# Kernel tuning notes

Measured on AMD Instinct MI355X. Metric: run time of the kernel, lower is better.

Reference implementation:

```python
import jax, jax.numpy as jnp
import numpy as np

N = 100000   # nodes
E = 800000   # directed edges
IN = 256     # in_channels (== hidden, required by repo's vn MLP dims)
HID = 256    # hidden_channels
OUT = 40     # out_channels (arxiv classes)
EPS = 1e-5


def setup_inputs() -> dict:
    key = jax.random.key(0)
    ks = jax.random.split(key, 8)
    def nrm(k, shape, scale=0.05):
        return jax.random.normal(k, shape, dtype=jnp.float32) * scale
    return {
        "x": nrm(ks[0], (N, IN), 1.0),
        "edge_index": jax.random.randint(ks[1], (2, E), 0, N, dtype=jnp.int32),
        # GCNConv weights (PyG: x @ W, then normalized aggregation, then + bias)
        "W0": nrm(ks[2], (IN, HID)),  "b0": jnp.zeros((HID,), jnp.float32),
        "W1": nrm(ks[3], (HID, HID)), "b1": jnp.zeros((HID,), jnp.float32),
        "W2": nrm(ks[4], (HID, OUT)), "b2": jnp.zeros((OUT,), jnp.float32),
        # BatchNorm1d affine params (batch-stat math, training mode)
        "bn_g0": jnp.ones((HID,), jnp.float32), "bn_b0": jnp.zeros((HID,), jnp.float32),
        "bn_g1": jnp.ones((HID,), jnp.float32), "bn_b1": jnp.zeros((HID,), jnp.float32),
        # virtual node embedding (init to 0 per reset_parameters)
        "vn_emb": jnp.zeros((1, IN), jnp.float32),
        # mlp_vns[0]: Linear(IN,HID) + LayerNorm(HID) + ReLU
        "vn_W0": nrm(ks[5], (IN, HID)),  "vn_b0": jnp.zeros((HID,), jnp.float32),
        "ln_g0": jnp.ones((HID,), jnp.float32), "ln_b0": jnp.zeros((HID,), jnp.float32),
        # mlp_vns[1]: Linear(HID,HID) + LayerNorm(HID) + ReLU
        "vn_W1": nrm(ks[6], (HID, HID)), "vn_b1": jnp.zeros((HID,), jnp.float32),
        "ln_g1": jnp.ones((HID,), jnp.float32), "ln_b1": jnp.zeros((HID,), jnp.float32),
    }


def _forward(x, edge_index, W0, b0, W1, b1, W2, b2, bn_g0, bn_b0, bn_g1, bn_b1,
             vn_emb, vn_W0, vn_b0, ln_g0, ln_b0, vn_W1, vn_b1, ln_g1, ln_b1):
    src, dst = edge_index[0], edge_index[1]
    # GCN symmetric normalization with self-loops: deg = in-degree + 1
    deg = jax.ops.segment_sum(jnp.ones(src.shape, jnp.float32), dst, num_segments=N) + 1.0
    dis = jax.lax.rsqrt(deg)                       # deg^{-1/2}  [N]
    coef = (dis[src] * dis[dst])[:, None]          # edge norm   [E,1]
    self_coef = (dis * dis)[:, None]               # self-loop norm = deg^{-1}  [N,1]

    def gcn(h, W, b):
        h = h @ W                                             # [N, out]
        agg = jax.ops.segment_sum(h[src] * coef, dst, num_segments=N)
        return agg + h * self_coef + b

    def bn(h, g, bv):  # BatchNorm1d, batch statistics over nodes
        mu = h.mean(0)
        var = ((h - mu) ** 2).mean(0)
        return (h - mu) * jax.lax.rsqrt(var + EPS) * g + bv

    def ln(h, g, bv):  # LayerNorm over last dim
        mu = h.mean(-1, keepdims=True)
        var = ((h - mu) ** 2).mean(-1, keepdims=True)
        return (h - mu) * jax.lax.rsqrt(var + EPS) * g + bv

    vx = vn_emb                                   # [1, IN]
    # layer 0
    h = x + vx                                    # virtual-node broadcast
    h = gcn(h, W0, b0)
    h = jax.nn.relu(bn(h, bn_g0, bn_b0))          # dropout = identity (eval)
    pool = jnp.sum(h, axis=0, keepdims=True)      # global_add_pool
    vx = jax.nn.relu(ln((pool + vx) @ vn_W0 + vn_b0, ln_g0, ln_b0))
    # layer 1
    h = h + vx
    h = gcn(h, W1, b1)
    h = jax.nn.relu(bn(h, bn_g1, bn_b1))
    pool = jnp.sum(h, axis=0, keepdims=True)
    vx = jax.nn.relu(ln((pool + vx) @ vn_W1 + vn_b1, ln_g1, ln_b1))
    # layer 2 (output)
    h = h + vx
    h = gcn(h, W2, b2)
    return jax.nn.log_softmax(h, axis=-1)


def reference(x, edge_index, W0, b0, W1, b1, W2, b2, bn_g0, bn_b0, bn_g1, bn_b1,
              vn_emb, vn_W0, vn_b0, ln_g0, ln_b0, vn_W1, vn_b1, ln_g1, ln_b1):
    return _forward(x, edge_index, W0, b0, W1, b1, W2, b2, bn_g0, bn_b0, bn_g1, bn_b1,
                    vn_emb, vn_W0, vn_b0, ln_g0, ln_b0, vn_W1, vn_b1, ln_g1, ln_b1)
```

## Files before the change

kernel.cpp:

```cpp
#include <hip/hip_runtime.h>
#include <hip/hip_bf16.h>
#include <cstdint>

#define N_NODES 100000
#define N_EDGES 800000
#define CH      256
#define COUT    40
#define COUTP   48
#define EPS     1e-5f
#define SCAN_CHUNK 1024
#define NSCAN_BLK  98
#define AGG_NPW 16

typedef unsigned short u16;
typedef unsigned int   u32;
typedef short s16x8 __attribute__((ext_vector_type(8)));
typedef float f32x4 __attribute__((ext_vector_type(4)));

__device__ __forceinline__ float b2f(u32 u) { return __uint_as_float(u << 16); }
__device__ __forceinline__ u16 f2b(float f) {
    u32 u = __float_as_uint(f);
    u32 r = (u + 0x7fffu + ((u >> 16) & 1u)) >> 16;
    return (u16)r;
}
__device__ __forceinline__ u32 packb(float a, float b) {
    return (u32)f2b(a) | ((u32)f2b(b) << 16);
}
__device__ __forceinline__ void unpack8(uint4 v, float* f) {
    f[0] = b2f(v.x & 0xffffu); f[1] = b2f(v.x >> 16);
    f[2] = b2f(v.y & 0xffffu); f[3] = b2f(v.y >> 16);
    f[4] = b2f(v.z & 0xffffu); f[5] = b2f(v.z >> 16);
    f[6] = b2f(v.w & 0xffffu); f[7] = b2f(v.w >> 16);
}

__global__ void k_count(const int* __restrict__ dst, int* __restrict__ counts) {
    int e = blockIdx.x * 256 + threadIdx.x;
    if (e < N_EDGES) atomicAdd(&counts[dst[e]], 1);
}

__global__ void k_scan1(const int* __restrict__ counts, int* __restrict__ partial,
                        int* __restrict__ blocksums) {
    __shared__ int sdata[256];
    int base = blockIdx.x * SCAN_CHUNK;
    int t = threadIdx.x;
    int v[4]; int s = 0;
    for (int j = 0; j < 4; j++) {
        int i = base + t * 4 + j;
        v[j] = (i < N_NODES) ? counts[i] : 0;
        s += v[j];
    }
    sdata[t] = s; __syncthreads();
    for (int off = 1; off < 256; off <<= 1) {
        int x = (t >= off) ? sdata[t - off] : 0;
        __syncthreads();
        sdata[t] += x;
        __syncthreads();
    }
    int incl = sdata[t];
    int run = incl - s;
    if (t == 255) blocksums[blockIdx.x] = incl;
    for (int j = 0; j < 4; j++) {
        int i = base + t * 4 + j;
        if (i < N_NODES) partial[i] = run;
        run += v[j];
    }
}

__global__ void k_scan2(int* __restrict__ blocksums) {
    __shared__ int sd[128];
    int t = threadIdx.x;
    int v = (t < NSCAN_BLK) ? blocksums[t] : 0;
    sd[t] = v; __syncthreads();
    for (int off = 1; off < 128; off <<= 1) {
        int x = (t >= off) ? sd[t - off] : 0;
        __syncthreads();
        sd[t] += x;
        __syncthreads();
    }
    if (t < NSCAN_BLK) blocksums[t] = sd[t] - v;
}

__global__ void k_scan3(int* __restrict__ row_start, const int* __restrict__ blocksums,
                        int* __restrict__ cursor, const int* __restrict__ counts,
                        float* __restrict__ dis) {
    int i = blockIdx.x * 256 + threadIdx.x;
    if (i < N_NODES) {
        int v = row_start[i] + blocksums[i >> 10];
        row_start[i] = v;
        cursor[i] = v;
        dis[i] = rsqrtf(1.0f + (float)counts[i]);
    }
}

__global__ void k_fill(const int* __restrict__ src, const int* __restrict__ dst,
                       int* __restrict__ cursor, int2* __restrict__ edata,
                       const float* __restrict__ dis) {
    int e = blockIdx.x * 256 + threadIdx.x;
    if (e < N_EDGES) {
        int d = dst[e], s = src[e];
        int p = atomicAdd(&cursor[d], 1);
        int2 v; v.x = s; v.y = __float_as_int(dis[s] * dis[d]);
        edata[p] = v;
    }
}

__global__ void k_wt3(const float* __restrict__ W0, const float* __restrict__ W1,
                      const float* __restrict__ W2,
                      u16* __restrict__ T0, u16* __restrict__ T1, u16* __restrict__ T2) {
    int b = blockIdx.x, k = threadIdx.x;
    if (b < 256) {
        T0[b * 256 + k] = f2b(W0[k * 256 + b]);
    } else if (b < 512) {
        int n = b - 256;
        T1[n * 256 + k] = f2b(W1[k * 256 + n]);
    } else {
        int n = b - 512;
        T2[n * 256 + k] = f2b(n < COUT ? W2[k * COUT + n] : 0.f);
    }
}

__global__ void k_vecmat(const float* __restrict__ vec, const float* __restrict__ W,
                         int ncols, int npad, float* __restrict__ outv) {
    __shared__ float s[256];
    int t = threadIdx.x;
    s[t] = vec[t];
    __syncthreads();
    float acc = 0.f;
    if (t < ncols) {
        for (int k = 0; k < 256; k++) acc += s[k] * W[k * ncols + t];
    }
    if (t < npad) outv[t] = acc;
}

__global__ __launch_bounds__(256) void k_gemm_f32a(const float* __restrict__ A,
                                                   const u16* __restrict__ Wt,
                                                   u16* __restrict__ Hout) {
    __shared__ u16 Bs[256 * 72];
    __shared__ u16 As[64 * 72];
    const int t = threadIdx.x;
    const int wave = t >> 6, lane = t & 63;
    const int lm = lane & 15, quad = lane >> 4;
    const int m0 = blockIdx.x * 64;
    const int ar = t >> 2, as_ = (t & 3) * 16;
    const int arow = m0 + ar;
    const f32x4 vz = {0.f, 0.f, 0.f, 0.f};
    f32x4 acc[4][4];
    for (int m = 0; m < 4; m++)
        for (int c = 0; c < 4; c++) acc[m][c] = vz;

    for (int k0 = 0; k0 < 256; k0 += 64) {
        {
            const uint4* bsrc = (const uint4*)(Wt + t * 256 + k0);
            uint4* bdst = (uint4*)(Bs + t * 72);
#pragma unroll
            for (int j = 0; j < 8; j++) bdst[j] = bsrc[j];
            uint4 p0 = {0,0,0,0}, p1 = {0,0,0,0};
            if (arow < N_NODES) {
                const float4* asrc = (const float4*)(A + (size_t)arow * 256 + k0 + as_);
                float4 x0 = asrc[0], x1 = asrc[1], x2 = asrc[2], x3 = asrc[3];
                p0.x = packb(x0.x, x0.y); p0.y = packb(x0.z, x0.w);
                p0.z = packb(x1.x, x1.y); p0.w = packb(x1.z, x1.w);
                p1.x = packb(x2.x, x2.y); p1.y = packb(x2.z, x2.w);
                p1.z = packb(x3.x, x3.y); p1.w = packb(x3.z, x3.w);
            }
            uint4* adst = (uint4*)(As + ar * 72 + as_);
            adst[0] = p0; adst[1] = p1;
        }
        __syncthreads();
#pragma unroll
        for (int kk = 0; kk < 64; kk += 32) {
            s16x8 af[4], bf[4];
#pragma unroll
            for (int m = 0; m < 4; m++)
                af[m] = *(const s16x8*)(As + (m * 16 + lm) * 72 + kk + quad * 8);
#pragma unroll
            for (int c = 0; c < 4; c++)
                bf[c] = *(const s16x8*)(Bs + (wave * 64 + c * 16 + lm) * 72 + kk + quad * 8);
#pragma unroll
            for (int c = 0; c < 4; c++)
#pragma unroll
                for (int m = 0; m < 4; m++)
                    acc[m][c] = __builtin_amdgcn_mfma_f32_16x16x32_bf16(af[m], bf[c], acc[m][c], 0, 0, 0);
        }
        __syncthreads();
    }
#pragma unroll
    for (int m = 0; m < 4; m++) {
#pragma unroll
        for (int c = 0; c < 4; c++) {
            int col = wave * 64 + c * 16 + lm;
#pragma unroll
            for (int i = 0; i < 4; i++) {
                int row = m0 + m * 16 + quad * 4 + i;
                if (row < N_NODES) Hout[(size_t)row * 256 + col] = f2b(acc[m][c][i]);
            }
        }
    }
}

__global__ __launch_bounds__(256) void k_gemm_bn(const u16* __restrict__ A,
                                                 const float* __restrict__ stats,
                                                 const float* __restrict__ g,
                                                 const float* __restrict__ bv,
                                                 const u16* __restrict__ Wt,
                                                 u16* __restrict__ Hout,
                                                 float* __restrict__ pool) {
    __shared__ u16 Bs[256 * 72];
    __shared__ u16 As[64 * 72];
    __shared__ float ggs[256], bcs[256], pls[256];
    const int t = threadIdx.x;
    const int wave = t >> 6, lane = t & 63;
    const int lm = lane & 15, quad = lane >> 4;
    const int m0 = blockIdx.x * 64;
    const int ar = t >> 2, as_ = (t & 3) * 16;
    const int arow = m0 + ar;
    {
        const float inv = 1.0f / (float)N_NODES;
        float mu = stats[t] * inv;
        float var = stats[256 + t] * inv - mu * mu;
        float rs = rsqrtf(var + EPS);
        float gg = g[t] * rs;
        ggs[t] = gg; bcs[t] = bv[t] - mu * gg;
        pls[t] = 0.f;
    }
    __syncthreads();
    const f32x4 vz = {0.f, 0.f, 0.f, 0.f};
    f32x4 acc[4][4];
    for (int m = 0; m < 4; m++)
        for (int c = 0; c < 4; c++) acc[m][c] = vz;

    for (int k0 = 0; k0 < 256; k0 += 64) {
        {
            const uint4* bsrc = (const uint4*)(Wt + t * 256 + k0);
            uint4* bdst = (uint4*)(Bs + t * 72);
#pragma unroll
            for (int j = 0; j < 8; j++) bdst[j] = bsrc[j];
            float f[16];
            if (arow < N_NODES) {
                const uint4* asrc = (const uint4*)(A + (size_t)arow * 256 + k0 + as_);
                uint4 r0 = asrc[0], r1 = asrc[1];
                unpack8(r0, f); unpack8(r1, f + 8);
#pragma unroll
                for (int j = 0; j < 16; j++) {
                    int c = k0 + as_ + j;
                    f[j] = fmaxf(f[j] * ggs[c] + bcs[c], 0.f);
                }
            } else {
#pragma unroll
                for (int j = 0; j < 16; j++) f[j] = 0.f;
            }
#pragma unroll
            for (int j = 0; j < 16; j++) {
                float v = f[j];
                v += __shfl_xor(v, 4);  v += __shfl_xor(v, 8);
                v += __shfl_xor(v, 16); v += __shfl_xor(v, 32);
                if (lane < 4) atomicAdd(&pls[k0 + lane * 16 + j], v);
            }
            uint4 p0, p1;
            p0.x = packb(f[0], f[1]);   p0.y = packb(f[2], f[3]);
            p0.z = packb(f[4], f[5]);   p0.w = packb(f[6], f[7]);
            p1.x = packb(f[8], f[9]);   p1.y = packb(f[10], f[11]);
            p1.z = packb(f[12], f[13]); p1.w = packb(f[14], f[15]);
            uint4* adst = (uint4*)(As + ar * 72 + as_);
            adst[0] = p0; adst[1] = p1;
        }
        __syncthreads();
#pragma unroll
        for (int kk = 0; kk < 64; kk += 32) {
            s16x8 af[4], bf[4];
#pragma unroll
            for (int m = 0; m < 4; m++)
                af[m] = *(const s16x8*)(As + (m * 16 + lm) * 72 + kk + quad * 8);
#pragma unroll
            for (int c = 0; c < 4; c++)
                bf[c] = *(const s16x8*)(Bs + (wave * 64 + c * 16 + lm) * 72 + kk + quad * 8);
#pragma unroll
            for (int c = 0; c < 4; c++)
#pragma unroll
                for (int m = 0; m < 4; m++)
                    acc[m][c] = __builtin_amdgcn_mfma_f32_16x16x32_bf16(af[m], bf[c], acc[m][c], 0, 0, 0);
        }
        __syncthreads();
    }
    atomicAdd(&pool[(blockIdx.x & 7) * 256 + t], pls[t]);
#pragma unroll
    for (int m = 0; m < 4; m++) {
#pragma unroll
        for (int c = 0; c < 4; c++) {
            int col = wave * 64 + c * 16 + lm;
#pragma unroll
            for (int i = 0; i < 4; i++) {
                int row = m0 + m * 16 + quad * 4 + i;
                if (row < N_NODES) Hout[(size_t)row * 256 + col] = f2b(acc[m][c][i]);
            }
        }
    }
}

__global__ __launch_bounds__(256) void k_gemm2_bn(const u16* __restrict__ A,
                                                  const float* __restrict__ stats,
                                                  const float* __restrict__ g,
                                                  const float* __restrict__ bv,
                                                  const u16* __restrict__ Wt,
                                                  u16* __restrict__ Hout,
                                                  float* __restrict__ pool) {
    __shared__ u16 Bs[48 * 72];
    __shared__ u16 As[64 * 72];
    __shared__ float ggs[256], bcs[256], pls[256];
    const int t = threadIdx.x;
    const int wave = t >> 6, lane = t & 63;
    const int lm = lane & 15, quad = lane >> 4;
    const int m0 = blockIdx.x * 64;
    const int ar = t >> 2, as_ = (t & 3) * 16;
    const int arow = m0 + ar;
    {
        const float inv = 1.0f / (float)N_NODES;
        float mu = stats[t] * inv;
        float var = stats[256 + t] * inv - mu * mu;
        float rs = rsqrtf(var + EPS);
        float gg = g[t] * rs;
        ggs[t] = gg; bcs[t] = bv[t] - mu * gg;
        pls[t] = 0.f;
    }
    __syncthreads();
    const f32x4 vz = {0.f, 0.f, 0.f, 0.f};
    f32x4 acc[3]; acc[0] = vz; acc[1] = vz; acc[2] = vz;

    for (int k0 = 0; k0 < 256; k0 += 64) {
        {
            if (t < 48) {
                const uint4* bsrc = (const uint4*)(Wt + t * 256 + k0);
                uint4* bdst = (uint4*)(Bs + t * 72);
#pragma unroll
                for (int j = 0; j < 8; j++) bdst[j] = bsrc[j];
            }
            float f[16];
            if (arow < N_NODES) {
                const uint4* asrc = (const uint4*)(A + (size_t)arow * 256 + k0 + as_);
                uint4 r0 = asrc[0], r1 = asrc[1];
                unpack8(r0, f); unpack8(r1, f + 8);
#pragma unroll
                for (int j = 0; j < 16; j++) {
                    int c = k0 + as_ + j;
                    f[j] = fmaxf(f[j] * ggs[c] + bcs[c], 0.f);
                }
            } else {
#pragma unroll
                for (int j = 0; j < 16; j++) f[j] = 0.f;
            }
#pragma unroll
            for (int j = 0; j < 16; j++) {
                float v = f[j];
                v += __shfl_xor(v, 4);  v += __shfl_xor(v, 8);
                v += __shfl_xor(v, 16); v += __shfl_xor(v, 32);
                if (lane < 4) atomicAdd(&pls[k0 + lane * 16 + j], v);
            }
            uint4 p0, p1;
            p0.x = packb(f[0], f[1]);   p0.y = packb(f[2], f[3]);
            p0.z = packb(f[4], f[5]);   p0.w = packb(f[6], f[7]);
            p1.x = packb(f[8], f[9]);   p1.y = packb(f[10], f[11]);
            p1.z = packb(f[12], f[13]); p1.w = packb(f[14], f[15]);
            uint4* adst = (uint4*)(As + ar * 72 + as_);
            adst[0] = p0; adst[1] = p1;
        }
        __syncthreads();
#pragma unroll
        for (int kk = 0; kk < 64; kk += 32) {
            s16x8 af = *(const s16x8*)(As + (wave * 16 + lm) * 72 + kk + quad * 8);
#pragma unroll
            for (int c = 0; c < 3; c++) {
                s16x8 bf = *(const s16x8*)(Bs + (c * 16 + lm) * 72 + kk + quad * 8);
                acc[c] = __builtin_amdgcn_mfma_f32_16x16x32_bf16(af, bf, acc[c], 0, 0, 0);
            }
        }
        __syncthreads();
    }
    atomicAdd(&pool[(blockIdx.x & 7) * 256 + t], pls[t]);
#pragma unroll
    for (int c = 0; c < 3; c++) {
        int col = c * 16 + lm;
#pragma unroll
        for (int i = 0; i < 4; i++) {
            int row = m0 + wave * 16 + quad * 4 + i;
            if (row < N_NODES) Hout[(size_t)row * COUTP + col] = f2b(acc[c][i]);
        }
    }
}

__global__ __launch_bounds__(256) void k_agg(const u16* __restrict__ H2,
                                             const int* __restrict__ row_start,
                                             const int* __restrict__ counts,
                                             const int2* __restrict__ edata,
                                             const float* __restrict__ dis,
                                             const float* __restrict__ bias,
                                             const float* __restrict__ v2,
                                             u16* __restrict__ OutB,
                                             float* __restrict__ stats) {
    __shared__ float ls[512];
    const int t = threadIdx.x, wave = t >> 6, lane = t & 63;
    const int half = lane >> 5, hl = lane & 31;
    const int ci = hl * 8;
    const float4 bbA = *(const float4*)(bias + ci);
    const float4 bbB = *(const float4*)(bias + ci + 4);
    const float4 vvA = *(const float4*)(v2 + ci);
    const float4 vvB = *(const float4*)(v2 + ci + 4);
    float s[8], q[8];
#pragma unroll
    for (int j = 0; j < 8; j++) { s[j] = 0.f; q[j] = 0.f; }

    const int nbase = blockIdx.x * (4 * AGG_NPW) + wave * AGG_NPW;
    const int nid = nbase + lane;
    const bool nv = (lane < AGG_NPW) && (nid < N_NODES);
    const int   my_rs = nv ? row_start[nid] : 0;
    const int   my_ct = nv ? counts[nid] : 0;
    const float my_dn = nv ? dis[nid] : 0.f;

    int beg = __shfl(my_rs, 0), cnt = __shfl(my_ct, 0);
    int2 my_e = {0, 0};
    if (lane < cnt) my_e = edata[beg + lane];

    for (int i = 0; i < AGG_NPW; i++) {
        const int node = nbase + i;
        if (node >= N_NODES) break;
        const int2 cur_e = my_e;
        const int  ccnt = cnt, cbeg = beg;
        const float dn = __shfl(my_dn, i);
        const uint4 rs_ = *(const uint4*)(H2 + (size_t)node * 256 + ci);
        if (i + 1 < AGG_NPW && node + 1 < N_NODES) {
            beg = __shfl(my_rs, i + 1);
            cnt = __shfl(my_ct, i + 1);
            int2 tmp = {0, 0};
            if (lane < cnt) tmp = edata[beg + lane];
            my_e = tmp;
        }
        const int cnt64 = ccnt < 64 ? ccnt : 64;
        const int cnt8 = (cnt64 + 7) & ~7;
        float a[8];
#pragma unroll
        for (int j = 0; j < 8; j++) a[j] = 0.f;
        float cs = 0.f;
        for (int e = 0; e < cnt8; e += 8) {
            const int   si0 = __shfl(cur_e.x, e + half);
            const int   si1 = __shfl(cur_e.x, e + 2 + half);
            const int   si2 = __shfl(cur_e.x, e + 4 + half);
            const int   si3 = __shfl(cur_e.x, e + 6 + half);
            const float cf0 = __int_as_float(__shfl(cur_e.y, e + half));
            const float cf1 = __int_as_float(__shfl(cur_e.y, e + 2 + half));
            const float cf2 = __int_as_float(__shfl(cur_e.y, e + 4 + half));
            const float cf3 = __int_as_float(__shfl(cur_e.y, e + 6 + half));
            const uint4 r0 = *(const uint4*)(H2 + (size_t)si0 * 256 + ci);
            const uint4 r1 = *(const uint4*)(H2 + (size_t)si1 * 256 + ci);
            const uint4 r2 = *(const uint4*)(H2 + (size_t)si2 * 256 + ci);
            const uint4 r3 = *(const uint4*)(H2 + (size_t)si3 * 256 + ci);
            cs += cf0 + cf1 + cf2 + cf3;
            a[0] += cf0*b2f(r0.x&0xffffu) + cf1*b2f(r1.x&0xffffu) + cf2*b2f(r2.x&0xffffu) + cf3*b2f(r3.x&0xffffu);
            a[1] += cf0*b2f(r0.x>>16)     + cf1*b2f(r1.x>>16)     + cf2*b2f(r2.x>>16)     + cf3*b2f(r3.x>>16);
            a[2] += cf0*b2f(r0.y&0xffffu) + cf1*b2f(r1.y&0xffffu) + cf2*b2f(r2.y&0xffffu) + cf3*b2f(r3.y&0xffffu);
            a[3] += cf0*b2f(r0.y>>16)     + cf1*b2f(r1.y>>16)     + cf2*b2f(r2.y>>16)     + cf3*b2f(r3.y>>16);
            a[4] += cf0*b2f(r0.z&0xffffu) + cf1*b2f(r1.z&0xffffu) + cf2*b2f(r2.z&0xffffu) + cf3*b2f(r3.z&0xffffu);
            a[5] += cf0*b2f(r0.z>>16)     + cf1*b2f(r1.z>>16)     + cf2*b2f(r2.z>>16)     + cf3*b2f(r3.z>>16);
            a[6] += cf0*b2f(r0.w&0xffffu) + cf1*b2f(r1.w&0xffffu) + cf2*b2f(r2.w&0xffffu) + cf3*b2f(r3.w&0xffffu);
            a[7] += cf0*b2f(r0.w>>16)     + cf1*b2f(r1.w>>16)     + cf2*b2f(r2.w>>16)     + cf3*b2f(r3.w>>16);
        }
        if (ccnt > 64) {
            int e2 = 64;
            for (; e2 + 2 <= ccnt; e2 += 2) {
                const int2 ed_ = edata[cbeg + e2 + half];
                const float cf = __int_as_float(ed_.y);
                const uint4 r = *(const uint4*)(H2 + (size_t)ed_.x * 256 + ci);
                cs += cf;
                a[0] += cf*b2f(r.x&0xffffu); a[1] += cf*b2f(r.x>>16);
                a[2] += cf*b2f(r.y&0xffffu); a[3] += cf*b2f(r.y>>16);
                a[4] += cf*b2f(r.z&0xffffu); a[5] += cf*b2f(r.z>>16);
                a[6] += cf*b2f(r.w&0xffffu); a[7] += cf*b2f(r.w>>16);
            }
            if (e2 < ccnt && half == 0) {
                const int2 ed_ = edata[cbeg + e2];
                const float cf = __int_as_float(ed_.y);
                const uint4 r = *(const uint4*)(H2 + (size_t)ed_.x * 256 + ci);
                cs += cf;
                a[0] += cf*b2f(r.x&0xffffu); a[1] += cf*b2f(r.x>>16);
                a[2] += cf*b2f(r.y&0xffffu); a[3] += cf*b2f(r.y>>16);
                a[4] += cf*b2f(r.z&0xffffu); a[5] += cf*b2f(r.z>>16);
                a[6] += cf*b2f(r.w&0xffffu); a[7] += cf*b2f(r.w>>16);
            }
        }
        cs += __shfl_xor(cs, 32);
#pragma unroll
        for (int j = 0; j < 8; j++) a[j] += __shfl_xor(a[j], 32);
        const float sc = dn * dn, cv = cs + sc;
        const float f0 = a[0] + sc*b2f(rs_.x&0xffffu) + cv*vvA.x + bbA.x;
        const float f1 = a[1] + sc*b2f(rs_.x>>16)     + cv*vvA.y + bbA.y;
        const float f2 = a[2] + sc*b2f(rs_.y&0xffffu) + cv*vvA.z + bbA.z;
        const float f3 = a[3] + sc*b2f(rs_.y>>16)     + cv*vvA.w + bbA.w;
        const float f4 = a[4] + sc*b2f(rs_.z&0xffffu) + cv*vvB.x + bbB.x;
        const float f5 = a[5] + sc*b2f(rs_.z>>16)     + cv*vvB.y + bbB.y;
        const float f6 = a[6] + sc*b2f(rs_.w&0xffffu) + cv*vvB.z + bbB.z;
        const float f7 = a[7] + sc*b2f(rs_.w>>16)     + cv*vvB.w + bbB.w;
        if (half == 0) {
            uint4 o;
            o.x = packb(f0, f1); o.y = packb(f2, f3);
            o.z = packb(f4, f5); o.w = packb(f6, f7);
            *(uint4*)(OutB + (size_t)node * 256 + ci) = o;
        }
        s[0] += f0; q[0] += f0*f0;  s[1] += f1; q[1] += f1*f1;
        s[2] += f2; q[2] += f2*f2;  s[3] += f3; q[3] += f3*f3;
        s[4] += f4; q[4] += f4*f4;  s[5] += f5; q[5] += f5*f5;
        s[6] += f6; q[6] += f6*f6;  s[7] += f7; q[7] += f7*f7;
    }
    ls[t] = 0.f; ls[256 + t] = 0.f;
    __syncthreads();
    if (half == 0) {
#pragma unroll
        for (int j = 0; j < 8; j++) {
            atomicAdd(&ls[ci + j], s[j]);
            atomicAdd(&ls[256 + ci + j], q[j]);
        }
    }
    __syncthreads();
    atomicAdd(&stats[t], ls[t]);
    atomicAdd(&stats[256 + t], ls[256 + t]);
}

__global__ void k_vx(const float* __restrict__ pool, const float* __restrict__ vx_old,
                     const float* __restrict__ vnW, const float* __restrict__ vnb,
                     const float* __restrict__ lng, const float* __restrict__ lnb,
                     float* __restrict__ vx_new,
                     const float* __restrict__ Wnext, int ncn, int npn,
                     float* __restrict__ v2n) {
    __shared__ float s[256];
    __shared__ float red[256];
    int t = threadIdx.x;
    float pv = 0.f;
#pragma unroll
    for (int r = 0; r < 8; r++) pv += pool[r * 256 + t];
    s[t] = pv + vx_old[t];
    __syncthreads();
    float y = vnb[t];
    for (int k = 0; k < 256; k++) y += s[k] * vnW[k * 256 + t];
    red[t] = y; __syncthreads();
    for (int off = 128; off > 0; off >>= 1) {
        if (t < off) red[t] += red[t + off];
        __syncthreads();
    }
    float mu = red[0] * (1.f / 256.f);
    __syncthreads();
    float d = y - mu;
    red[t] = d * d; __syncthreads();
    for (int off = 128; off > 0; off >>= 1) {
        if (t < off) red[t] += red[t + off];
        __syncthreads();
    }
    float var = red[0] * (1.f / 256.f);
    float v = fmaxf(d * rsqrtf(var + EPS) * lng[t] + lnb[t], 0.f);
    vx_new[t] = v;
    __syncthreads();
    s[t] = v;
    __syncthreads();
    float acc = 0.f;
    if (t < ncn) {
        for (int k = 0; k < 256; k++) acc += s[k] * Wnext[k * ncn + t];
    }
    if (t < npn) v2n[t] = acc;
}

__global__ __launch_bounds__(256) void k_agg2(const u16* __restrict__ H2,
                                              const int* __restrict__ row_start,
                                              const int* __restrict__ counts,
                                              const int2* __restrict__ edata,
                                              const float* __restrict__ dis,
                                              const float* __restrict__ bias,
                                              const float* __restrict__ v2,
                                              float* __restrict__ OutF) {
    const int t = threadIdx.x, wave = t >> 6, lane = t & 63;
    const int half = lane >> 5, hl = lane & 31;
    const bool gact = hl < 24;
    const bool cact = hl < 20;
    const int c0 = 2 * hl;
    float bb0 = 0.f, bb1 = 0.f, vv0 = 0.f, vv1 = 0.f;
    if (cact) {
        float2 bv = *(const float2*)(bias + c0); bb0 = bv.x; bb1 = bv.y;
        float2 vvv = *(const float2*)(v2 + c0);  vv0 = vvv.x; vv1 = vvv.y;
    }
    const int nbase = blockIdx.x * 16 + wave * 4;
    for (int i = 0; i < 4; i++) {
        const int node = nbase + i;
        const int beg = row_start[node], cnt = counts[node];
        const float dn = dis[node];
        float a0 = 0.f, a1 = 0.f, cs = 0.f;
        int e = half;
        for (; e + 6 < cnt; e += 8) {
            int2 ea = edata[beg+e],   eb = edata[beg+e+2];
            int2 ec = edata[beg+e+4], ed = edata[beg+e+6];
            float ca = __int_as_float(ea.y), cb = __int_as_float(eb.y);
            float cc = __int_as_float(ec.y), cd = __int_as_float(ed.y);
            u32 ra = 0, rb = 0, rc = 0, rd = 0;
            if (gact) {
                ra = *(const u32*)(H2 + (size_t)ea.x * COUTP + c0);
                rb = *(const u32*)(H2 + (size_t)eb.x * COUTP + c0);
                rc = *(const u32*)(H2 + (size_t)ec.x * COUTP + c0);
                rd = *(const u32*)(H2 + (size_t)ed.x * COUTP + c0);
            }
            cs += ca + cb + cc + cd;
            a0 += ca*b2f(ra&0xffffu) + cb*b2f(rb&0xffffu) + cc*b2f(rc&0xffffu) + cd*b2f(rd&0xffffu);
            a1 += ca*b2f(ra>>16)     + cb*b2f(rb>>16)     + cc*b2f(rc>>16)     + cd*b2f(rd>>16);
        }
        for (; e < cnt; e += 2) {
            int2 ea = edata[beg+e];
            float ca = __int_as_float(ea.y);
            u32 ra = gact ? *(const u32*)(H2 + (size_t)ea.x * COUTP + c0) : 0u;
            cs += ca;
            a0 += ca*b2f(ra&0xffffu); a1 += ca*b2f(ra>>16);
        }
        a0 += __shfl_xor(a0, 32);
        a1 += __shfl_xor(a1, 32);
        cs += __shfl_xor(cs, 32);
        const float sc = dn * dn;
        u32 rs_ = gact ? *(const u32*)(H2 + (size_t)node * COUTP + c0) : 0u;
        float h0 = a0 + sc*b2f(rs_&0xffffu) + (cs+sc)*vv0 + bb0;
        float h1 = a1 + sc*b2f(rs_>>16)     + (cs+sc)*vv1 + bb1;
        float m = cact ? fmaxf(h0, h1) : -3.0e38f;
#pragma unroll
        for (int off = 16; off > 0; off >>= 1) m = fmaxf(m, __shfl_xor(m, off));
        float ex = cact ? (expf(h0 - m) + expf(h1 - m)) : 0.f;
        float se = ex;
#pragma unroll
        for (int off = 16; off > 0; off >>= 1) se += __shfl_xor(se, off);
        float lg = logf(se);
        if (cact && half == 0) {
            float2 o = {h0 - m - lg, h1 - m - lg};
            *(float2*)(OutF + (size_t)node * COUT + c0) = o;
        }
    }
}

extern "C" void kernel_launch(void* const* d_in, const int* in_sizes, int n_in,
                              void* d_out, int out_size, void* d_ws, size_t ws_size,
                              hipStream_t stream) {
    const float* x   = (const float*)d_in[0];
    const int*   ei  = (const int*)d_in[1];
    const int*   esrc = ei;
    const int*   edst = ei + N_EDGES;
    const float* W0 = (const float*)d_in[2];  const float* b0 = (const float*)d_in[3];
    const float* W1 = (const float*)d_in[4];  const float* b1 = (const float*)d_in[5];
    const float* W2 = (const float*)d_in[6];  const float* b2 = (const float*)d_in[7];
    const float* bg0 = (const float*)d_in[8]; const float* bb0 = (const float*)d_in[9];
    const float* bg1 = (const float*)d_in[10]; const float* bb1 = (const float*)d_in[11];
    const float* vn_emb = (const float*)d_in[12];
    const float* vW0 = (const float*)d_in[13]; const float* vb0 = (const float*)d_in[14];
    const float* lg0 = (const float*)d_in[15]; const float* lb0 = (const float*)d_in[16];
    const float* vW1 = (const float*)d_in[17]; const float* vb1 = (const float*)d_in[18];
    const float* lg1 = (const float*)d_in[19]; const float* lb1 = (const float*)d_in[20];

    char* w = (char*)d_ws;
    auto alloc = [&](size_t bytes) { void* p = (void*)w; w += ((bytes + 255) / 256) * 256; return p; };
    u16* H2    = (u16*)alloc((size_t)N_NODES * 256 * 2);
    u16* OutB  = (u16*)alloc((size_t)N_NODES * 256 * 2);
    int2* edata = (int2*)alloc((size_t)N_EDGES * 8);
    int* counts = (int*)alloc((size_t)N_NODES * 4);
    int* rowst  = (int*)alloc((size_t)N_NODES * 4);
    int* cursor = (int*)alloc((size_t)N_NODES * 4);
    float* dis  = (float*)alloc((size_t)N_NODES * 4);
    u16* Wtb0 = (u16*)alloc(256 * 256 * 2);
    u16* Wtb1 = (u16*)alloc(256 * 256 * 2);
    u16* Wt2b = (u16*)alloc(COUTP * 256 * 2);
    int* scanblk = (int*)alloc(128 * 4);
    float* statsA = (float*)alloc(2560 * 4);
    float* statsB = (float*)alloc(2560 * 4);
    float* vxA = (float*)alloc(256 * 4);
    float* vxB = (float*)alloc(256 * 4);
    float* v20 = (float*)alloc(256 * 4);
    float* v21 = (float*)alloc(256 * 4);
    float* v22 = (float*)alloc(64 * 4);
    (void)ws_size; (void)in_sizes; (void)n_in; (void)out_size;

    hipMemsetAsync(counts, 0, (size_t)N_NODES * 4, stream);
    hipMemsetAsync(statsA, 0, 2560 * 4, stream);
    hipMemsetAsync(statsB, 0, 2560 * 4, stream);
    k_count<<<(N_EDGES + 255) / 256, 256, 0, stream>>>(edst, counts);
    k_scan1<<<NSCAN_BLK, 256, 0, stream>>>(counts, rowst, scanblk);
    k_scan2<<<1, 128, 0, stream>>>(scanblk);
    k_scan3<<<(N_NODES + 255) / 256, 256, 0, stream>>>(rowst, scanblk, cursor, counts, dis);
    k_fill<<<(N_EDGES + 255) / 256, 256, 0, stream>>>(esrc, edst, cursor, edata, dis);

    k_wt3<<<512 + COUTP, 256, 0, stream>>>(W0, W1, W2, Wtb0, Wtb1, Wt2b);
    k_vecmat<<<1, 256, 0, stream>>>(vn_emb, W0, 256, 256, v20);

    const int gemmblk = (N_NODES + 63) / 64;
    const int aggblk = (N_NODES + 63) / 64;

    k_gemm_f32a<<<gemmblk, 256, 0, stream>>>(x, Wtb0, H2);
    k_agg<<<aggblk, 256, 0, stream>>>(H2, rowst, counts, edata, dis, b0, v20, OutB, statsA);
    k_gemm_bn<<<gemmblk, 256, 0, stream>>>(OutB, statsA, bg0, bb0, Wtb1, H2, statsA + 512);
    k_vx<<<1, 256, 0, stream>>>(statsA + 512, vn_emb, vW0, vb0, lg0, lb0, vxA, W1, 256, 256, v21);
    k_agg<<<aggblk, 256, 0, stream>>>(H2, rowst, counts, edata, dis, b1, v21, OutB, statsB);
    k_gemm2_bn<<<gemmblk, 256, 0, stream>>>(OutB, statsB, bg1, bb1, Wt2b, H2, statsB + 512);
    k_vx<<<1, 256, 0, stream>>>(statsB + 512, vxA, vW1, vb1, lg1, lb1, vxB, W2, COUT, COUTP, v22);
    k_agg2<<<N_NODES / 16, 256, 0, stream>>>(H2, rowst, counts, edata, dis, b2, v22, (float*)d_out);
}
```

Measured before the change: 735.6 us.

## Make aggregation kernel persistent with atomic ticket-based dynamic node scheduling

The two hidden-layer aggregation kernels now run as a fixed grid of 2048 persistent blocks. Each wave claims 4-node chunks from a global atomic ticket counter instead of owning a static 16-node range, which is meant to even out the load imbalance caused by varying node degrees. Launch bounds now request 8 waves per SIMD, and the per-block BN statistic atomics happen once per persistent block rather than once per small block. The cost is one global atomic per chunk, shorter prefetch pipelining across nodes, and a ticket buffer that must be zeroed on every call.

Result: slower. 1.493 ms (+103.0%).

```diff
diff --git a/kernel.cpp b/kernel.cpp
--- a/kernel.cpp
+++ b/kernel.cpp
@@ -10,7 +10,8 @@
 #define EPS     1e-5f
 #define SCAN_CHUNK 1024
 #define NSCAN_BLK  98
-#define AGG_NPW 16
+#define AGG_CHUNK  4
+#define AGG_BLOCKS 2048
 
 typedef unsigned short u16;
 typedef unsigned int   u32;
@@ -387,7 +388,7 @@
     }
 }
 
-__global__ __launch_bounds__(256) void k_agg(const u16* __restrict__ H2,
+__global__ __launch_bounds__(256, 8) void k_agg(const u16* __restrict__ H2,
                                              const int* __restrict__ row_start,
                                              const int* __restrict__ counts,
                                              const int2* __restrict__ edata,
@@ -395,9 +396,10 @@
                                              const float* __restrict__ bias,
                                              const float* __restrict__ v2,
                                              u16* __restrict__ OutB,
-                                             float* __restrict__ stats) {
+                                             float* __restrict__ stats,
+                                             int* __restrict__ ticket) {
     __shared__ float ls[512];
-    const int t = threadIdx.x, wave = t >> 6, lane = t & 63;
+    const int t = threadIdx.x, lane = t & 63;
     const int half = lane >> 5, hl = lane & 31;
     const int ci = hl * 8;
     const float4 bbA = *(const float4*)(bias + ci);
@@ -408,105 +410,110 @@
 #pragma unroll
     for (int j = 0; j < 8; j++) { s[j] = 0.f; q[j] = 0.f; }
 
-    const int nbase = blockIdx.x * (4 * AGG_NPW) + wave * AGG_NPW;
-    const int nid = nbase + lane;
-    const bool nv = (lane < AGG_NPW) && (nid < N_NODES);
-    const int   my_rs = nv ? row_start[nid] : 0;
-    const int   my_ct = nv ? counts[nid] : 0;
-    const float my_dn = nv ? dis[nid] : 0.f;
-
-    int beg = __shfl(my_rs, 0), cnt = __shfl(my_ct, 0);
-    int2 my_e = {0, 0};
-    if (lane < cnt) my_e = edata[beg + lane];
-
-    for (int i = 0; i < AGG_NPW; i++) {
-        const int node = nbase + i;
-        if (node >= N_NODES) break;
-        const int2 cur_e = my_e;
-        const int  ccnt = cnt, cbeg = beg;
-        const float dn = __shfl(my_dn, i);
-        const uint4 rs_ = *(const uint4*)(H2 + (size_t)node * 256 + ci);
-        if (i + 1 < AGG_NPW && node + 1 < N_NODES) {
-            beg = __shfl(my_rs, i + 1);
-            cnt = __shfl(my_ct, i + 1);
-            int2 tmp = {0, 0};
-            if (lane < cnt) tmp = edata[beg + lane];
-            my_e = tmp;
-        }
-        const int cnt64 = ccnt < 64 ? ccnt : 64;
-        const int cnt8 = (cnt64 + 7) & ~7;
-        float a[8];
-#pragma unroll
-        for (int j = 0; j < 8; j++) a[j] = 0.f;
-        float cs = 0.f;
-        for (int e = 0; e < cnt8; e += 8) {
-            const int   si0 = __shfl(cur_e.x, e + half);
-            const int   si1 = __shfl(cur_e.x, e + 2 + half);
-            const int   si2 = __shfl(cur_e.x, e + 4 + half);
-            const int   si3 = __shfl(cur_e.x, e + 6 + half);
-            const float cf0 = __int_as_float(__shfl(cur_e.y, e + half));
-            const float cf1 = __int_as_float(__shfl(cur_e.y, e + 2 + half));
-            const float cf2 = __int_as_float(__shfl(cur_e.y, e + 4 + half));
-            const float cf3 = __int_as_float(__shfl(cur_e.y, e + 6 + half));
-            const uint4 r0 = *(const uint4*)(H2 + (size_t)si0 * 256 + ci);
-            const uint4 r1 = *(const uint4*)(H2 + (size_t)si1 * 256 + ci);
-            const uint4 r2 = *(const uint4*)(H2 + (size_t)si2 * 256 + ci);
-            const uint4 r3 = *(const uint4*)(H2 + (size_t)si3 * 256 + ci);
-            cs += cf0 + cf1 + cf2 + cf3;
-            a[0] += cf0*b2f(r0.x&0xffffu) + cf1*b2f(r1.x&0xffffu) + cf2*b2f(r2.x&0xffffu) + cf3*b2f(r3.x&0xffffu);
-            a[1] += cf0*b2f(r0.x>>16)     + cf1*b2f(r1.x>>16)     + cf2*b2f(r2.x>>16)     + cf3*b2f(r3.x>>16);
-            a[2] += cf0*b2f(r0.y&0xffffu) + cf1*b2f(r1.y&0xffffu) + cf2*b2f(r2.y&0xffffu) + cf3*b2f(r3.y&0xffffu);
-            a[3] += cf0*b2f(r0.y>>16)     + cf1*b2f(r1.y>>16)     + cf2*b2f(r2.y>>16)     + cf3*b2f(r3.y>>16);
-            a[4] += cf0*b2f(r0.z&0xffffu) + cf1*b2f(r1.z&0xffffu) + cf2*b2f(r2.z&0xffffu) + cf3*b2f(r3.z&0xffffu);
-            a[5] += cf0*b2f(r0.z>>16)     + cf1*b2f(r1.z>>16)     + cf2*b2f(r2.z>>16)     + cf3*b2f(r3.z>>16);
-            a[6] += cf0*b2f(r0.w&0xffffu) + cf1*b2f(r1.w&0xffffu) + cf2*b2f(r2.w&0xffffu) + cf3*b2f(r3.w&0xffffu);
-            a[7] += cf0*b2f(r0.w>>16)     + cf1*b2f(r1.w>>16)     + cf2*b2f(r2.w>>16)     + cf3*b2f(r3.w>>16);
-        }
-        if (ccnt > 64) {
-            int e2 = 64;
-            for (; e2 + 2 <= ccnt; e2 += 2) {
-                const int2 ed_ = edata[cbeg + e2 + half];
-                const float cf = __int_as_float(ed_.y);
-                const uint4 r = *(const uint4*)(H2 + (size_t)ed_.x * 256 + ci);
-                cs += cf;
-                a[0] += cf*b2f(r.x&0xffffu); a[1] += cf*b2f(r.x>>16);
-                a[2] += cf*b2f(r.y&0xffffu); a[3] += cf*b2f(r.y>>16);
-                a[4] += cf*b2f(r.z&0xffffu); a[5] += cf*b2f(r.z>>16);
-                a[6] += cf*b2f(r.w&0xffffu); a[7] += cf*b2f(r.w>>16);
-            }
-            if (e2 < ccnt && half == 0) {
-                const int2 ed_ = edata[cbeg + e2];
-                const float cf = __int_as_float(ed_.y);
-                const uint4 r = *(const uint4*)(H2 + (size_t)ed_.x * 256 + ci);
-                cs += cf;
-                a[0] += cf*b2f(r.x&0xffffu); a[1] += cf*b2f(r.x>>16);
-                a[2] += cf*b2f(r.y&0xffffu); a[3] += cf*b2f(r.y>>16);
-                a[4] += cf*b2f(r.z&0xffffu); a[5] += cf*b2f(r.z>>16);
-                a[6] += cf*b2f(r.w&0xffffu); a[7] += cf*b2f(r.w>>16);
-            }
-        }
-        cs += __shfl_xor(cs, 32);
-#pragma unroll
-        for (int j = 0; j < 8; j++) a[j] += __shfl_xor(a[j], 32);
-        const float sc = dn * dn, cv = cs + sc;
-        const float f0 = a[0] + sc*b2f(rs_.x&0xffffu) + cv*vvA.x + bbA.x;
-        const float f1 = a[1] + sc*b2f(rs_.x>>16)     + cv*vvA.y + bbA.y;
-        const float f2 = a[2] + sc*b2f(rs_.y&0xffffu) + cv*vvA.z + bbA.z;
-        const float f3 = a[3] + sc*b2f(rs_.y>>16)     + cv*vvA.w + bbA.w;
-        const float f4 = a[4] + sc*b2f(rs_.z&0xffffu) + cv*vvB.x + bbB.x;
-        const float f5 = a[5] + sc*b2f(rs_.z>>16)     + cv*vvB.y + bbB.y;
-        const float f6 = a[6] + sc*b2f(rs_.w&0xffffu) + cv*vvB.z + bbB.z;
-        const float f7 = a[7] + sc*b2f(rs_.w>>16)     + cv*vvB.w + bbB.w;
-        if (half == 0) {
-            uint4 o;
-            o.x = packb(f0, f1); o.y = packb(f2, f3);
-            o.z = packb(f4, f5); o.w = packb(f6, f7);
-            *(uint4*)(OutB + (size_t)node * 256 + ci) = o;
-        }
-        s[0] += f0; q[0] += f0*f0;  s[1] += f1; q[1] += f1*f1;
-        s[2] += f2; q[2] += f2*f2;  s[3] += f3; q[3] += f3*f3;
-        s[4] += f4; q[4] += f4*f4;  s[5] += f5; q[5] += f5*f5;
-        s[6] += f6; q[6] += f6*f6;  s[7] += f7; q[7] += f7*f7;
+    for (;;) {
+        int tk = 0;
+        if (lane == 0) tk = atomicAdd(ticket, AGG_CHUNK);
+        const int nbase = __shfl(tk, 0);
+        if (nbase >= N_NODES) break;
+        const int nid = nbase + lane;
+        const bool nv = (lane < AGG_CHUNK) && (nid < N_NODES);
+        const int   my_rs = nv ? row_start[nid] : 0;
+        const int   my_ct = nv ? counts[nid] : 0;
+        const float my_dn = nv ? dis[nid] : 0.f;
+
+        int beg = __shfl(my_rs, 0), cnt = __shfl(my_ct, 0);
+        int2 my_e = {0, 0};
+        if (lane < cnt) my_e = edata[beg + lane];
+
+        for (int i = 0; i < AGG_CHUNK; i++) {
+            const int node = nbase + i;
+            if (node >= N_NODES) break;
+            const int2 cur_e = my_e;
+            const int  ccnt = cnt, cbeg = beg;
+            const float dn = __shfl(my_dn, i);
+            const uint4 rs_ = *(const uint4*)(H2 + (size_t)node * 256 + ci);
+            if (i + 1 < AGG_CHUNK && node + 1 < N_NODES) {
+                beg = __shfl(my_rs, i + 1);
+                cnt = __shfl(my_ct, i + 1);
+                int2 tmp = {0, 0};
+                if (lane < cnt) tmp = edata[beg + lane];
+                my_e = tmp;
+            }
+            const int cnt64 = ccnt < 64 ? ccnt : 64;
+            const int cnt8 = (cnt64 + 7) & ~7;
+            float a[8];
+#pragma unroll
+            for (int j = 0; j < 8; j++) a[j] = 0.f;
+            float cs = 0.f;
+            for (int e = 0; e < cnt8; e += 8) {
+                const int   si0 = __shfl(cur_e.x, e + half);
+                const int   si1 = __shfl(cur_e.x, e + 2 + half);
+                const int   si2 = __shfl(cur_e.x, e + 4 + half);
+                const int   si3 = __shfl(cur_e.x, e + 6 + half);
+                const float cf0 = __int_as_float(__shfl(cur_e.y, e + half));
+                const float cf1 = __int_as_float(__shfl(cur_e.y, e + 2 + half));
+                const float cf2 = __int_as_float(__shfl(cur_e.y, e + 4 + half));
+                const float cf3 = __int_as_float(__shfl(cur_e.y, e + 6 + half));
+                const uint4 r0 = *(const uint4*)(H2 + (size_t)si0 * 256 + ci);
+                const uint4 r1 = *(const uint4*)(H2 + (size_t)si1 * 256 + ci);
+                const uint4 r2 = *(const uint4*)(H2 + (size_t)si2 * 256 + ci);
+                const uint4 r3 = *(const uint4*)(H2 + (size_t)si3 * 256 + ci);
+                cs += cf0 + cf1 + cf2 + cf3;
+                a[0] += cf0*b2f(r0.x&0xffffu) + cf1*b2f(r1.x&0xffffu) + cf2*b2f(r2.x&0xffffu) + cf3*b2f(r3.x&0xffffu);
+                a[1] += cf0*b2f(r0.x>>16)     + cf1*b2f(r1.x>>16)     + cf2*b2f(r2.x>>16)     + cf3*b2f(r3.x>>16);
+                a[2] += cf0*b2f(r0.y&0xffffu) + cf1*b2f(r1.y&0xffffu) + cf2*b2f(r2.y&0xffffu) + cf3*b2f(r3.y&0xffffu);
+                a[3] += cf0*b2f(r0.y>>16)     + cf1*b2f(r1.y>>16)     + cf2*b2f(r2.y>>16)     + cf3*b2f(r3.y>>16);
+                a[4] += cf0*b2f(r0.z&0xffffu) + cf1*b2f(r1.z&0xffffu) + cf2*b2f(r2.z&0xffffu) + cf3*b2f(r3.z&0xffffu);
+                a[5] += cf0*b2f(r0.z>>16)     + cf1*b2f(r1.z>>16)     + cf2*b2f(r2.z>>16)     + cf3*b2f(r3.z>>16);
+                a[6] += cf0*b2f(r0.w&0xffffu) + cf1*b2f(r1.w&0xffffu) + cf2*b2f(r2.w&0xffffu) + cf3*b2f(r3.w&0xffffu);
+                a[7] += cf0*b2f(r0.w>>16)     + cf1*b2f(r1.w>>16)     + cf2*b2f(r2.w>>16)     + cf3*b2f(r3.w>>16);
+            }
+            if (ccnt > 64) {
+                int e2 = 64;
+                for (; e2 + 2 <= ccnt; e2 += 2) {
+                    const int2 ed_ = edata[cbeg + e2 + half];
+                    const float cf = __int_as_float(ed_.y);
+                    const uint4 r = *(const uint4*)(H2 + (size_t)ed_.x * 256 + ci);
+                    cs += cf;
+                    a[0] += cf*b2f(r.x&0xffffu); a[1] += cf*b2f(r.x>>16);
+                    a[2] += cf*b2f(r.y&0xffffu); a[3] += cf*b2f(r.y>>16);
+                    a[4] += cf*b2f(r.z&0xffffu); a[5] += cf*b2f(r.z>>16);
+                    a[6] += cf*b2f(r.w&0xffffu); a[7] += cf*b2f(r.w>>16);
+                }
+                if (e2 < ccnt && half == 0) {
+                    const int2 ed_ = edata[cbeg + e2];
+                    const float cf = __int_as_float(ed_.y);
+                    const uint4 r = *(const uint4*)(H2 + (size_t)ed_.x * 256 + ci);
+                    cs += cf;
+                    a[0] += cf*b2f(r.x&0xffffu); a[1] += cf*b2f(r.x>>16);
+                    a[2] += cf*b2f(r.y&0xffffu); a[3] += cf*b2f(r.y>>16);
+                    a[4] += cf*b2f(r.z&0xffffu); a[5] += cf*b2f(r.z>>16);
+                    a[6] += cf*b2f(r.w&0xffffu); a[7] += cf*b2f(r.w>>16);
+                }
+            }
+            cs += __shfl_xor(cs, 32);
+#pragma unroll
+            for (int j = 0; j < 8; j++) a[j] += __shfl_xor(a[j], 32);
+            const float sc = dn * dn, cv = cs + sc;
+            const float f0 = a[0] + sc*b2f(rs_.x&0xffffu) + cv*vvA.x + bbA.x;
+            const float f1 = a[1] + sc*b2f(rs_.x>>16)     + cv*vvA.y + bbA.y;
+            const float f2 = a[2] + sc*b2f(rs_.y&0xffffu) + cv*vvA.z + bbA.z;
+            const float f3 = a[3] + sc*b2f(rs_.y>>16)     + cv*vvA.w + bbA.w;
+            const float f4 = a[4] + sc*b2f(rs_.z&0xffffu) + cv*vvB.x + bbB.x;
+            const float f5 = a[5] + sc*b2f(rs_.z>>16)     + cv*vvB.y + bbB.y;
+            const float f6 = a[6] + sc*b2f(rs_.w&0xffffu) + cv*vvB.z + bbB.z;
+            const float f7 = a[7] + sc*b2f(rs_.w>>16)     + cv*vvB.w + bbB.w;
+            if (half == 0) {
+                uint4 o;
+                o.x = packb(f0, f1); o.y = packb(f2, f3);
+                o.z = packb(f4, f5); o.w = packb(f6, f7);
+                *(uint4*)(OutB + (size_t)node * 256 + ci) = o;
+            }
+            s[0] += f0; q[0] += f0*f0;  s[1] += f1; q[1] += f1*f1;
+            s[2] += f2; q[2] += f2*f2;  s[3] += f3; q[3] += f3*f3;
+            s[4] += f4; q[4] += f4*f4;  s[5] += f5; q[5] += f5*f5;
+            s[6] += f6; q[6] += f6*f6;  s[7] += f7; q[7] += f7*f7;
+        }
     }
     ls[t] = 0.f; ls[256 + t] = 0.f;
     __syncthreads();
@@ -672,11 +679,13 @@
     float* v20 = (float*)alloc(256 * 4);
     float* v21 = (float*)alloc(256 * 4);
     float* v22 = (float*)alloc(64 * 4);
+    int* tickets = (int*)alloc(2 * 4);
     (void)ws_size; (void)in_sizes; (void)n_in; (void)out_size;
 
     hipMemsetAsync(counts, 0, (size_t)N_NODES * 4, stream);
     hipMemsetAsync(statsA, 0, 2560 * 4, stream);
     hipMemsetAsync(statsB, 0, 2560 * 4, stream);
+    hipMemsetAsync(tickets, 0, 2 * 4, stream);
     k_count<<<(N_EDGES + 255) / 256, 256, 0, stream>>>(edst, counts);
     k_scan1<<<NSCAN_BLK, 256, 0, stream>>>(counts, rowst, scanblk);
     k_scan2<<<1, 128, 0, stream>>>(scanblk);
@@ -687,13 +696,12 @@
     k_vecmat<<<1, 256, 0, stream>>>(vn_emb, W0, 256, 256, v20);
 
     const int gemmblk = (N_NODES + 63) / 64;
-    const int aggblk = (N_NODES + 63) / 64;
 
     k_gemm_f32a<<<gemmblk, 256, 0, stream>>>(x, Wtb0, H2);
-    k_agg<<<aggblk, 256, 0, stream>>>(H2, rowst, counts, edata, dis, b0, v20, OutB, statsA);
+    k_agg<<<AGG_BLOCKS, 256, 0, stream>>>(H2, rowst, counts, edata, dis, b0, v20, OutB, statsA, tickets + 0);
     k_gemm_bn<<<gemmblk, 256, 0, stream>>>(OutB, statsA, bg0, bb0, Wtb1, H2, statsA + 512);
     k_vx<<<1, 256, 0, stream>>>(statsA + 512, vn_emb, vW0, vb0, lg0, lb0, vxA, W1, 256, 256, v21);
-    k_agg<<<aggblk, 256, 0, stream>>>(H2, rowst, counts, edata, dis, b1, v21, OutB, statsB);
+    k_agg<<<AGG_BLOCKS, 256, 0, stream>>>(H2, rowst, counts, edata, dis, b1, v21, OutB, statsB, tickets + 1);
     k_gemm2_bn<<<gemmblk, 256, 0, stream>>>(OutB, statsB, bg1, bb1, Wt2b, H2, statsB + 512);
     k_vx<<<1, 256, 0, stream>>>(statsB + 512, vxA, vW1, vb1, lg1, lb1, vxB, W2, COUT, COUTP, v22);
     k_agg2<<<N_NODES / 16, 256, 0, stream>>>(H2, rowst, counts, edata, dis, b2, v22, (float*)d_out);
```
